# Kernel tuning notes

Measured on AMD Instinct MI355X. Metric: run time of the kernel, lower is better.

The kernel has to match this reference:

```python
import jax, jax.numpy as jnp
import numpy as np

B, T, E, H = 2, 4096, 1024, 16
D = E // H
EPS = 1e-6


def setup_inputs() -> dict:
    key = jax.random.key(0)
    ks = jax.random.split(key, 9)
    s = 1.0 / np.sqrt(E)
    return {
        "x": jax.random.normal(ks[0], (B, T, E), dtype=jnp.float32),
        "wq": jax.random.uniform(ks[1], (E, E), jnp.float32, -s, s),
        "bq": jax.random.uniform(ks[2], (E,), jnp.float32, -s, s),
        "wk": jax.random.uniform(ks[3], (E, E), jnp.float32, -s, s),
        "bk": jax.random.uniform(ks[4], (E,), jnp.float32, -s, s),
        "wv": jax.random.uniform(ks[5], (E, E), jnp.float32, -s, s),
        "bv": jax.random.uniform(ks[6], (E,), jnp.float32, -s, s),
        "wo": jax.random.uniform(ks[7], (E, E), jnp.float32, -s, s),
        "bo": jax.random.uniform(ks[8], (E,), jnp.float32, -s, s),
    }


def _feature_map(x):
    # elu(x) + 1
    return jnp.where(x > 0, x + 1.0, jnp.exp(x))


def reference(x, wq, bq, wk, bk, wv, bv, wo, bo):
    b, t, e = x.shape
    q = _feature_map(x @ wq + bq).reshape(b, t, H, D)
    k = _feature_map(x @ wk + bk).reshape(b, t, H, D)
    v = (x @ wv + bv).reshape(b, t, H, D)

    # time-major for the recurrence: [T, B, H, D]
    qT = jnp.moveaxis(q, 1, 0)
    kT = jnp.moveaxis(k, 1, 0)
    vT = jnp.moveaxis(v, 1, 0)

    S0 = jnp.zeros((b, H, D, D), dtype=x.dtype)  # running sum of k \otimes v
    z0 = jnp.zeros((b, H, D), dtype=x.dtype)     # running sum of k

    def step(carry, qkv):
        S, z = carry
        qt, kt, vt = qkv
        S = S + jnp.einsum('bhd,bhe->bhde', kt, vt)
        z = z + kt
        num = jnp.einsum('bhd,bhde->bhe', qt, S)
        den = jnp.einsum('bhd,bhd->bh', qt, z)[..., None] + EPS
        return (S, z), num / den

    _, outT = jax.lax.scan(step, (S0, z0), (qT, kT, vT))  # [T, B, H, D]
    out = jnp.moveaxis(outT, 0, 1).reshape(b, t, e)
    return out @ wo + bo
```

## Files before the change

kernel.cpp:

```cpp
#include <hip/hip_runtime.h>
#include <hip/hip_bf16.h>
#include <cstdint>
#include <cstddef>

#define B_   2
#define T_   4096
#define E_   1024
#define H_   16
#define D_   64
#define M_   (B_ * T_)
#define KDIM 1024
#define NDIM 1024
#define EPSC 1e-6f
#define CT   128
#define NC   (T_ / CT)

typedef __attribute__((ext_vector_type(8))) short bf16x8;
typedef __attribute__((ext_vector_type(4))) float f32x4;

__device__ __forceinline__ float bf2f(uint32_t u) {
    union { uint32_t u; float f; } x; x.u = u << 16; return x.f;
}
__device__ __forceinline__ unsigned short f2bf(float f) {
    union { float f; uint32_t u; } x; x.f = f;
    uint32_t r = x.u + 0x7fffu + ((x.u >> 16) & 1u);
    return (unsigned short)(r >> 16);
}
__device__ __forceinline__ void gload16(const void* g, void* l) {
    __builtin_amdgcn_global_load_lds(
        (const __attribute__((address_space(1))) void*)g,
        (__attribute__((address_space(3))) void*)l, 16, 0, 0);
}

__global__ __launch_bounds__(256) void conv_bf16(
    const float* __restrict__ in, unsigned short* __restrict__ out)
{
    const int i = blockIdx.x * 256 + threadIdx.x;
    const float4* p = (const float4*)in;
    float4 a = p[i * 2], b = p[i * 2 + 1];
    ushort4 o0 = make_ushort4(f2bf(a.x), f2bf(a.y), f2bf(a.z), f2bf(a.w));
    ushort4 o1 = make_ushort4(f2bf(b.x), f2bf(b.y), f2bf(b.z), f2bf(b.w));
    *(ushort4*)&out[(size_t)i * 8] = o0;
    *(ushort4*)&out[(size_t)i * 8 + 4] = o1;
}

__global__ __launch_bounds__(256) void transpose_w4(
    const float* __restrict__ w0, const float* __restrict__ w1,
    const float* __restrict__ w2, const float* __restrict__ w3,
    unsigned short* __restrict__ o0, unsigned short* __restrict__ o1,
    unsigned short* __restrict__ o2, unsigned short* __restrict__ o3)
{
    const float* src; unsigned short* dst;
    switch (blockIdx.z) {
        case 0: src = w0; dst = o0; break;
        case 1: src = w1; dst = o1; break;
        case 2: src = w2; dst = o2; break;
        default: src = w3; dst = o3; break;
    }
    __shared__ float tile[64][65];
    const int t = threadIdx.x, tx = t & 63, ty = t >> 6;
    const int r0 = blockIdx.y * 64, c0 = blockIdx.x * 64;
#pragma unroll
    for (int i = 0; i < 16; ++i)
        tile[ty + i * 4][tx] = src[(size_t)(r0 + ty + i * 4) * KDIM + c0 + tx];
    __syncthreads();
#pragma unroll
    for (int i = 0; i < 16; ++i)
        dst[(size_t)(c0 + ty + i * 4) * KDIM + r0 + tx] = f2bf(tile[tx][ty + i * 4]);
}

__global__ __launch_bounds__(512, 2) void gemm_qkv3(
    const unsigned short* __restrict__ A,
    const unsigned short* __restrict__ Wt,
    const float* __restrict__ bq, const float* __restrict__ bk,
    const float* __restrict__ bv,
    unsigned short* __restrict__ qb,  unsigned short* __restrict__ kb,
    unsigned short* __restrict__ ktb, unsigned short* __restrict__ vtb)
{
    __shared__ char lds[98304];

    const int tid  = threadIdx.x;
    const int lane = tid & 63;
    const int w    = tid >> 6;
    const int wm   = w >> 2;
    const int wn   = w & 3;
    const int lo   = lane & 15, hi = lane >> 4;

    const int orig = blockIdx.x;
    const int swz  = (orig & 7) * 48 + (orig >> 3);
    const int bx = swz % 12;
    const int by = swz / 12;
    const int row0 = by * 256;
    const int col0 = bx * 256;

    const unsigned short* pa0; const unsigned short* pa1;
    const unsigned short* pb0; const unsigned short* pb1;
    {
        int X, Y, r, ko;
        X = tid * 16;           Y = X ^ (((X >> 9) & 1) << 5);
        r = ((Y >> 10) << 4) + ((Y >> 6) & 15);  ko = (Y & 63) >> 1;
        pa0 = A  + (size_t)(row0 + r) * KDIM + ko;
        pb0 = Wt + (size_t)(col0 + r) * KDIM + ko;
        X = (512 + tid) * 16;   Y = X ^ (((X >> 9) & 1) << 5);
        r = ((Y >> 10) << 4) + ((Y >> 6) & 15);  ko = (Y & 63) >> 1;
        pa1 = A  + (size_t)(row0 + r) * KDIM + ko;
        pb1 = Wt + (size_t)(col0 + r) * KDIM + ko;
    }
    const int woff = w * 1024;

    const int rdb = lo * 64 + hi * 16;
    const int fragoff = rdb ^ (((rdb >> 9) & 1) << 5);

#define LDSA(b) (lds + (b) * 16384)
#define LDSB(b) (lds + 49152 + (b) * 16384)
#define STAGE_A(t, b) { gload16(pa0 + (t) * 32, LDSA(b) + woff); \
                        gload16(pa1 + (t) * 32, LDSA(b) + 8192 + woff); }
#define STAGE_B(t, b) { gload16(pb0 + (t) * 32, LDSB(b) + woff); \
                        gload16(pb1 + (t) * 32, LDSB(b) + 8192 + woff); }

    f32x4 acc[8][4] = {};
    const int NT = KDIM / 32;

    STAGE_A(0, 0); STAGE_B(0, 0);
    STAGE_A(1, 1); STAGE_B(1, 1);
    asm volatile("s_waitcnt vmcnt(4)" ::: "memory");
    __builtin_amdgcn_s_barrier();

    for (int t = 0; t < NT; ++t) {
        const int cb = t % 3;
        const char* bufA = LDSA(cb);
        const char* bufB = LDSB(cb);
        const int nb = (t + 2) % 3;
        const bool more = (t + 2 < NT);

        if (more) STAGE_A(t + 2, nb);
        bf16x8 bfr[4], af[4];
#pragma unroll
        for (int n = 0; n < 4; ++n)
            bfr[n] = *(const bf16x8*)(bufB + (wn * 4 + n) * 1024 + fragoff);
#pragma unroll
        for (int m = 0; m < 4; ++m)
            af[m] = *(const bf16x8*)(bufA + (wm * 8 + m) * 1024 + fragoff);
        asm volatile("s_waitcnt lgkmcnt(0)" ::: "memory");
        __builtin_amdgcn_sched_barrier(0);
        __builtin_amdgcn_s_setprio(1);
#pragma unroll
        for (int m = 0; m < 4; ++m)
#pragma unroll
            for (int n = 0; n < 4; ++n)
                acc[m][n] = __builtin_amdgcn_mfma_f32_16x16x32_bf16(
                    af[m], bfr[n], acc[m][n], 0, 0, 0);
        __builtin_amdgcn_s_setprio(0);

        if (more) STAGE_B(t + 2, nb);
        bf16x8 af2[4];
#pragma unroll
        for (int m = 0; m < 4; ++m)
            af2[m] = *(const bf16x8*)(bufA + (wm * 8 + 4 + m) * 1024 + fragoff);
        asm volatile("s_waitcnt lgkmcnt(0)" ::: "memory");
        __builtin_amdgcn_sched_barrier(0);
        __builtin_amdgcn_s_setprio(1);
#pragma unroll
        for (int m = 0; m < 4; ++m)
#pragma unroll
            for (int n = 0; n < 4; ++n)
                acc[4 + m][n] = __builtin_amdgcn_mfma_f32_16x16x32_bf16(
                    af2[m], bfr[n], acc[4 + m][n], 0, 0, 0);
        __builtin_amdgcn_s_setprio(0);

        if (more) asm volatile("s_waitcnt vmcnt(4)" ::: "memory");
        else      asm volatile("s_waitcnt vmcnt(0)" ::: "memory");
        __builtin_amdgcn_s_barrier();
    }
#undef STAGE_A
#undef STAGE_B
#undef LDSA
#undef LDSB

    const int matid = bx >> 2;
    const int lcol0 = (bx & 3) * 256;
    const float* bias = (matid == 0) ? bq : (matid == 1) ? bk : bv;
    const int fcol = lane & 15, frow4 = (lane >> 4) * 4;
#pragma unroll
    for (int m = 0; m < 8; ++m) {
#pragma unroll
        for (int n = 0; n < 4; ++n) {
            const int lcol = lcol0 + wn * 64 + n * 16 + fcol;
            const float bval = bias[lcol];
            const int rbase = row0 + wm * 128 + m * 16 + frow4;
            const int h = lcol >> 6, d = lcol & 63;
            const int bb = rbase >> 12;
            const int tt = rbase & (T_ - 1);
            float vv[4];
#pragma unroll
            for (int j = 0; j < 4; ++j) {
                float v = acc[m][n][j] + bval;
                if (matid <= 1) v = (v > 0.f) ? (v + 1.f) : __expf(v);
                vv[j] = v;
            }
            if (matid == 0) {
#pragma unroll
                for (int j = 0; j < 4; ++j)
                    qb[((((size_t)bb * H_ + h) * T_) + tt + j) * D_ + d] = f2bf(vv[j]);
            } else if (matid == 1) {
#pragma unroll
                for (int j = 0; j < 4; ++j)
                    kb[((((size_t)bb * H_ + h) * T_) + tt + j) * D_ + d] = f2bf(vv[j]);
                ushort4 tp = make_ushort4(f2bf(vv[0]), f2bf(vv[1]),
                                          f2bf(vv[2]), f2bf(vv[3]));
                *(ushort4*)&ktb[(((size_t)bb * H_ + h) * D_ + d) * T_ + tt] = tp;
            } else {
                ushort4 tp = make_ushort4(f2bf(vv[0]), f2bf(vv[1]),
                                          f2bf(vv[2]), f2bf(vv[3]));
                *(ushort4*)&vtb[(((size_t)bb * H_ + h) * D_ + d) * T_ + tt] = tp;
            }
        }
    }
}

__global__ __launch_bounds__(256) void gemm_out(
    const unsigned short* __restrict__ A,
    const unsigned short* __restrict__ Bt,
    const float* __restrict__ bias, float* __restrict__ outf)
{
    __shared__ unsigned short As[128 * 32];
    __shared__ unsigned short Bs[128 * 32];

    const int tid  = threadIdx.x;
    const int lane = tid & 63;
    const int wave = tid >> 6;
    const int wr = wave >> 1, wc = wave & 1;
    const int orig = blockIdx.x;
    const int swz  = (orig & 7) * 64 + (orig >> 3);
    const int bx = swz & 7, by = swz >> 3;
    const int row0 = by * 128;
    const int col0 = bx * 128;

    f32x4 acc[4][4] = {};

    const unsigned short* Ag = A  + (size_t)(row0 + (tid >> 2)) * KDIM + (tid & 3) * 8;
    const unsigned short* Bg = Bt + (size_t)(col0 + (tid >> 2)) * KDIM + (tid & 3) * 8;
    unsigned short* AsW = As + wave * 512;
    unsigned short* BsW = Bs + wave * 512;

    const int fr = lane & 15;
    const int fk = (lane >> 4) * 8;

    for (int k0 = 0; k0 < KDIM; k0 += 32) {
        gload16(Ag + k0,              AsW);
        gload16(Ag + 64 * KDIM + k0,  AsW + 2048);
        gload16(Bg + k0,              BsW);
        gload16(Bg + 64 * KDIM + k0,  BsW + 2048);
        __syncthreads();

        bf16x8 af[4], bfr[4];
#pragma unroll
        for (int m = 0; m < 4; ++m)
            af[m] = *(const bf16x8*)&As[(wr * 64 + m * 16 + fr) * 32 + fk];
#pragma unroll
        for (int n = 0; n < 4; ++n)
            bfr[n] = *(const bf16x8*)&Bs[(wc * 64 + n * 16 + fr) * 32 + fk];
#pragma unroll
        for (int m = 0; m < 4; ++m)
#pragma unroll
            for (int n = 0; n < 4; ++n)
                acc[m][n] = __builtin_amdgcn_mfma_f32_16x16x32_bf16(
                    af[m], bfr[n], acc[m][n], 0, 0, 0);
        __syncthreads();
    }

    const int fcol = lane & 15;
    const int frow = (lane >> 4) * 4;
#pragma unroll
    for (int m = 0; m < 4; ++m) {
#pragma unroll
        for (int n = 0; n < 4; ++n) {
            const int col = col0 + wc * 64 + n * 16 + fcol;
            const float bval = bias[col];
            const int rbase = row0 + wr * 64 + m * 16 + frow;
#pragma unroll
            for (int j = 0; j < 4; ++j)
                outf[(size_t)(rbase + j) * NDIM + col] = acc[m][n][j] + bval;
        }
    }
}

__global__ __launch_bounds__(256) void chunk_sums_mfma(
    const unsigned short* __restrict__ Kt,
    const unsigned short* __restrict__ Vt,
    unsigned short* __restrict__ Sl,
    unsigned short* __restrict__ Zl)
{
    const int tid = threadIdx.x, lane = tid & 63, w = tid >> 6;
    const int lo = lane & 15, hi = lane >> 4;
    const int cid = blockIdx.x, bh = cid >> 5, c = cid & 31, t0 = c * CT;
    const unsigned short* kT = Kt + (size_t)bh * 64 * T_ + t0;
    const unsigned short* vT = Vt + (size_t)bh * 64 * T_ + t0;

    const bf16x8 ones8 = {0x3F80, 0x3F80, 0x3F80, 0x3F80,
                          0x3F80, 0x3F80, 0x3F80, 0x3F80};
    f32x4 acc[5] = {};
#pragma unroll
    for (int kt = 0; kt < 4; ++kt) {
        bf16x8 af = *(const bf16x8*)&kT[(size_t)(w * 16 + lo) * T_ + kt * 32 + hi * 8];
        bf16x8 bfr[5];
#pragma unroll
        for (int et = 0; et < 4; ++et)
            bfr[et] = *(const bf16x8*)&vT[(size_t)(et * 16 + lo) * T_ + kt * 32 + hi * 8];
        bfr[4] = ones8;
#pragma unroll
        for (int et = 0; et < 5; ++et)
            acc[et] = __builtin_amdgcn_mfma_f32_16x16x32_bf16(af, bfr[et], acc[et], 0, 0, 0);
    }
    unsigned short* sO = Sl + (size_t)cid * 4096;
    const int d0 = w * 16 + hi * 4;
#pragma unroll
    for (int et = 0; et < 4; ++et) {
        const int e = et * 16 + lo;
        ushort4 pk = make_ushort4(f2bf(acc[et][0]), f2bf(acc[et][1]),
                                  f2bf(acc[et][2]), f2bf(acc[et][3]));
        *(ushort4*)&sO[e * 64 + d0] = pk;
    }
    if (lo == 0) {
        ushort4 pk = make_ushort4(f2bf(acc[4][0]), f2bf(acc[4][1]),
                                  f2bf(acc[4][2]), f2bf(acc[4][3]));
        *(ushort4*)&Zl[(size_t)cid * 64 + d0] = pk;
    }
}

__global__ __launch_bounds__(256) void chunk_scan_bf(
    unsigned short* __restrict__ S, unsigned short* __restrict__ Z)
{
    const int bh = blockIdx.y;
    const int f0 = blockIdx.x * 512 + threadIdx.x * 2;
    float a0 = 0.f, a1 = 0.f;
    unsigned short* base = S + (size_t)bh * NC * 4096 + f0;
    for (int c = 0; c < NC; ++c) {
        uint32_t* p = (uint32_t*)(base + (size_t)c * 4096);
        uint32_t v = *p;
        float c0 = bf2f(v & 0xffffu), c1 = bf2f(v >> 16);
        *p = (uint32_t)f2bf(a0) | ((uint32_t)f2bf(a1) << 16);
        a0 += c0; a1 += c1;
    }
    if (blockIdx.x == 0 && threadIdx.x < 32) {
        float b0 = 0.f, b1 = 0.f;
        unsigned short* zb = Z + (size_t)bh * NC * 64 + threadIdx.x * 2;
        for (int c = 0; c < NC; ++c) {
            uint32_t* p = (uint32_t*)(zb + (size_t)c * 64);
            uint32_t v = *p;
            float c0 = bf2f(v & 0xffffu), c1 = bf2f(v >> 16);
            *p = (uint32_t)f2bf(b0) | ((uint32_t)f2bf(b1) << 16);
            b0 += c0; b1 += c1;
        }
    }
}

__global__ __launch_bounds__(256) void chunk_attn_mfma(
    const unsigned short* __restrict__ Qb,
    const unsigned short* __restrict__ Kb,
    const unsigned short* __restrict__ Vt,
    const unsigned short* __restrict__ SpT,
    const unsigned short* __restrict__ Zp,
    unsigned short* __restrict__ att)
{
    __shared__ unsigned short lds[128 * 128];

    const int tid = threadIdx.x;
    const int lane = tid & 63;
    const int w = tid >> 6;
    const int lo = lane & 15, hi = lane >> 4;
    const int cid = blockIdx.x;
    const int bh = cid >> 5, c = cid & 31;
    const int t0 = c * CT;

    const unsigned short* qB = Qb + ((size_t)bh * T_ + t0) * 64;
    const unsigned short* kB = Kb + ((size_t)bh * T_ + t0) * 64;
    const unsigned short* vB = Vt + (size_t)bh * 64 * T_ + t0;
    const unsigned short* sB = SpT + (size_t)cid * 4096;
    const unsigned short* zB = Zp + (size_t)cid * 64;

    bf16x8 ka[2][2];
#pragma unroll
    for (int si = 0; si < 2; ++si)
#pragma unroll
        for (int kt = 0; kt < 2; ++kt)
            ka[si][kt] = *(const bf16x8*)&kB[(w * 32 + si * 16 + lo) * 64 + kt * 32 + hi * 8];

    f32x4 pacc[2][8] = {};
#pragma unroll
    for (int ti = 0; ti < 8; ++ti) {
        if (ti >= 2 * w) {
#pragma unroll
            for (int kt = 0; kt < 2; ++kt) {
                bf16x8 qf = *(const bf16x8*)&qB[(ti * 16 + lo) * 64 + kt * 32 + hi * 8];
                pacc[0][ti] = __builtin_amdgcn_mfma_f32_16x16x32_bf16(
                    ka[0][kt], qf, pacc[0][ti], 0, 0, 0);
                if (ti >= 2 * w + 1)
                    pacc[1][ti] = __builtin_amdgcn_mfma_f32_16x16x32_bf16(
                        ka[1][kt], qf, pacc[1][ti], 0, 0, 0);
            }
        }
    }
#pragma unroll
    for (int ti = 0; ti < 8; ++ti) {
        if (ti >= 2 * w) {
            const int t = ti * 16 + lo;
#pragma unroll
            for (int si = 0; si < 2; ++si) {
                const int s0 = w * 32 + si * 16 + hi * 4;
                ushort4 pk;
                unsigned short* pe = (unsigned short*)&pk;
#pragma unroll
                for (int j = 0; j < 4; ++j)
                    pe[j] = (s0 + j <= t) ? f2bf(pacc[si][ti][j]) : (unsigned short)0;
                *(ushort4*)((char*)lds + t * 256 + ((s0 * 2) ^ ((t & 7) << 4))) = pk;
            }
        }
    }
    __syncthreads();

    const bf16x8 ones8 = {0x3F80, 0x3F80, 0x3F80, 0x3F80,
                          0x3F80, 0x3F80, 0x3F80, 0x3F80};
    f32x4 acc[2][5] = {};
#pragma unroll
    for (int kt = 0; kt < 6; ++kt) {
        const int skt = kt - 2;
        if (kt < 2 || skt <= w) {
            bf16x8 bfr[5];
            if (kt < 2) {
#pragma unroll
                for (int et = 0; et < 4; ++et)
                    bfr[et] = *(const bf16x8*)&sB[(et * 16 + lo) * 64 + kt * 32 + hi * 8];
                bfr[4] = *(const bf16x8*)&zB[kt * 32 + hi * 8];
            } else {
#pragma unroll
                for (int et = 0; et < 4; ++et)
                    bfr[et] = *(const bf16x8*)&vB[(size_t)(et * 16 + lo) * T_ + skt * 32 + hi * 8];
                bfr[4] = ones8;
            }
#pragma unroll
            for (int m = 0; m < 2; ++m) {
                const int t = w * 32 + m * 16 + lo;
                bf16x8 af;
                if (kt < 2)
                    af = *(const bf16x8*)&qB[t * 64 + kt * 32 + hi * 8];
                else
                    af = *(const bf16x8*)((char*)lds + t * 256 +
                         (((skt * 32 + hi * 8) * 2) ^ ((t & 7) << 4)));
#pragma unroll
                for (int et = 0; et < 5; ++et)
                    acc[m][et] = __builtin_amdgcn_mfma_f32_16x16x32_bf16(
                        af, bfr[et], acc[m][et], 0, 0, 0);
            }
        }
    }

    __syncthreads();
#pragma unroll
    for (int m = 0; m < 2; ++m) {
#pragma unroll
        for (int j = 0; j < 4; ++j) {
            const int t = w * 32 + m * 16 + hi * 4 + j;
            const float rden = 1.f / (acc[m][4][j] + EPSC);
#pragma unroll
            for (int et = 0; et < 4; ++et) {
                const int e = et * 16 + lo;
                *(unsigned short*)((char*)lds + t * 144 + e * 2) =
                    f2bf(acc[m][et][j] * rden);
            }
        }
    }
    __syncthreads();
    const int b = bh >> 4, h = bh & 15;
#pragma unroll
    for (int r = 0; r < 4; ++r) {
        const int vid = tid + r * 256;
        const int t = vid >> 3, eg = vid & 7;
        uint4 val = *(const uint4*)((const char*)lds + t * 144 + eg * 16);
        *(uint4*)&att[(size_t)(b * T_ + t0 + t) * E_ + h * 64 + eg * 8] = val;
    }
}

extern "C" void kernel_launch(void* const* d_in, const int* in_sizes, int n_in,
                              void* d_out, int out_size, void* d_ws, size_t ws_size,
                              hipStream_t stream)
{
    const float* x  = (const float*)d_in[0];
    const float* wq = (const float*)d_in[1];
    const float* bq = (const float*)d_in[2];
    const float* wk = (const float*)d_in[3];
    const float* bk = (const float*)d_in[4];
    const float* wv = (const float*)d_in[5];
    const float* bv = (const float*)d_in[6];
    const float* wo = (const float*)d_in[7];
    const float* bo = (const float*)d_in[8];
    float* out = (float*)d_out;

    char* ws = (char*)d_ws;
    unsigned short* qb  = (unsigned short*)(ws);
    unsigned short* kb  = (unsigned short*)(ws + (size_t)16 * 1024 * 1024);
    unsigned short* ktb = (unsigned short*)(ws + (size_t)32 * 1024 * 1024);
    unsigned short* vtb = (unsigned short*)(ws + (size_t)48 * 1024 * 1024);
    unsigned short* xb  = (unsigned short*)(ws + (size_t)64 * 1024 * 1024);
    unsigned short* attb = xb;
    unsigned short* Sl  = (unsigned short*)(ws + (size_t)80 * 1024 * 1024);
    unsigned short* Zl  = (unsigned short*)(ws + (size_t)88 * 1024 * 1024);
    unsigned short* wqT = (unsigned short*)(ws + (size_t)88 * 1024 * 1024 + 128 * 1024);
    unsigned short* wkT = wqT + (size_t)KDIM * NDIM;
    unsigned short* wvT = wkT + (size_t)KDIM * NDIM;
    unsigned short* woT = wvT + (size_t)KDIM * NDIM;

    conv_bf16<<<M_ * KDIM / (256 * 8), 256, 0, stream>>>(x, xb);
    transpose_w4<<<dim3(16, 16, 4), 256, 0, stream>>>(wq, wk, wv, wo,
                                                      wqT, wkT, wvT, woT);

    gemm_qkv3<<<384, 512, 0, stream>>>(xb, wqT, bq, bk, bv, qb, kb, ktb, vtb);

    chunk_sums_mfma<<<B_ * H_ * NC, 256, 0, stream>>>(ktb, vtb, Sl, Zl);
    chunk_scan_bf<<<dim3(8, B_ * H_), 256, 0, stream>>>(Sl, Zl);
    chunk_attn_mfma<<<B_ * H_ * NC, 256, 0, stream>>>(qb, kb, vtb, Sl, Zl, attb);

    gemm_out<<<512, 256, 0, stream>>>(attb, woT, bo, out);
}
```

Before: 171.1 us.

## Rework QKV GEMM mainloop to K=64 double-buffered tiles with interleaved prefetch

Restructures the fused QKV projection GEMM to process K in steps of 64 instead of 32, using two 64 KB double buffers (128 KB LDS) in place of a 3-stage ring of 32-wide tiles. The LDS layout changes to 128-byte rows with an XOR swizzle on bank-conflicting bits. The global-to-LDS loads for the next B tile and the A tile two steps ahead are split into halves and interleaved between four MFMA groups. The aim is to halve the per-K-step barrier and waitcnt overhead and hide load latency better. It raises LDS use to 128 KB per block, which may limit occupancy to one block per CU despite launch_bounds(512,2), and adds an extra mid-iteration barrier.

```diff
diff --git a/kernel.cpp b/kernel.cpp
--- a/kernel.cpp
+++ b/kernel.cpp
@@ -69,7 +69,7 @@
         dst[(size_t)(c0 + ty + i * 4) * KDIM + r0 + tx] = f2bf(tile[tx][ty + i * 4]);
 }
 
-__global__ __launch_bounds__(512, 2) void gemm_qkv3(
+__global__ __launch_bounds__(512, 2) void gemm_qkv8(
     const unsigned short* __restrict__ A,
     const unsigned short* __restrict__ Wt,
     const float* __restrict__ bq, const float* __restrict__ bk,
@@ -77,7 +77,7 @@
     unsigned short* __restrict__ qb,  unsigned short* __restrict__ kb,
     unsigned short* __restrict__ ktb, unsigned short* __restrict__ vtb)
 {
-    __shared__ char lds[98304];
+    __shared__ char lds[131072];
 
     const int tid  = threadIdx.x;
     const int lane = tid & 63;
@@ -93,99 +93,115 @@
     const int row0 = by * 256;
     const int col0 = bx * 256;
 
-    const unsigned short* pa0; const unsigned short* pa1;
-    const unsigned short* pb0; const unsigned short* pb1;
-    {
-        int X, Y, r, ko;
-        X = tid * 16;           Y = X ^ (((X >> 9) & 1) << 5);
-        r = ((Y >> 10) << 4) + ((Y >> 6) & 15);  ko = (Y & 63) >> 1;
-        pa0 = A  + (size_t)(row0 + r) * KDIM + ko;
-        pb0 = Wt + (size_t)(col0 + r) * KDIM + ko;
-        X = (512 + tid) * 16;   Y = X ^ (((X >> 9) & 1) << 5);
-        r = ((Y >> 10) << 4) + ((Y >> 6) & 15);  ko = (Y & 63) >> 1;
-        pa1 = A  + (size_t)(row0 + r) * KDIM + ko;
-        pb1 = Wt + (size_t)(col0 + r) * KDIM + ko;
-    }
-    const int woff = w * 1024;
-
-    const int rdb = lo * 64 + hi * 16;
-    const int fragoff = rdb ^ (((rdb >> 9) & 1) << 5);
-
-#define LDSA(b) (lds + (b) * 16384)
-#define LDSB(b) (lds + 49152 + (b) * 16384)
-#define STAGE_A(t, b) { gload16(pa0 + (t) * 32, LDSA(b) + woff); \
-                        gload16(pa1 + (t) * 32, LDSA(b) + 8192 + woff); }
-#define STAGE_B(t, b) { gload16(pb0 + (t) * 32, LDSB(b) + woff); \
-                        gload16(pb1 + (t) * 32, LDSB(b) + 8192 + woff); }
-
-    f32x4 acc[8][4] = {};
-    const int NT = KDIM / 32;
-
-    STAGE_A(0, 0); STAGE_B(0, 0);
-    STAGE_A(1, 1); STAGE_B(1, 1);
+    int sr0, sk0, sr1, sk1;
+    { int X = tid * 16;         int Y = X ^ (((X >> 7) & 7) << 4);
+      sr0 = Y >> 7; sk0 = (Y & 127) >> 1; }
+    { int X = (512 + tid) * 16; int Y = X ^ (((X >> 7) & 7) << 4);
+      sr1 = Y >> 7; sk1 = (Y & 127) >> 1; }
+    const unsigned short* sA0 = A  + (size_t)(row0 + sr0) * KDIM + sk0;
+    const unsigned short* sA1 = A  + (size_t)(row0 + sr1) * KDIM + sk1;
+    const unsigned short* sB0 = Wt + (size_t)(col0 + sr0) * KDIM + sk0;
+    const unsigned short* sB1 = Wt + (size_t)(col0 + sr1) * KDIM + sk1;
+
+#define BUFA(p) (lds + (p) * 32768)
+#define BUFB(p) (lds + 65536 + (p) * 32768)
+#define STGA(t, h) { char* d_ = BUFA((t) & 1) + (h) * 16384 + w * 1024;      \
+        gload16(sA0 + (size_t)(h) * 128 * KDIM + (t) * 64, d_);              \
+        gload16(sA1 + (size_t)(h) * 128 * KDIM + (t) * 64, d_ + 8192); }
+#define STGB(t, h) { char* d_ = BUFB((t) & 1) + (h) * 16384 + w * 1024;      \
+        gload16(sB0 + (size_t)(h) * 128 * KDIM + (t) * 64, d_);              \
+        gload16(sB1 + (size_t)(h) * 128 * KDIM + (t) * 64, d_ + 8192); }
+
+    const int koff0 = (hi * 16)      ^ ((lane & 7) << 4);
+    const int koff1 = (64 + hi * 16) ^ ((lane & 7) << 4);
+
+    f32x4  acc[8][4] = {};
+    bf16x8 af[8][2], bfr[4][2];
+
+#define MFMA_PAIR(mb) {                                                       \
+    _Pragma("unroll") for (int kk = 0; kk < 2; ++kk)                          \
+    _Pragma("unroll") for (int n = 0; n < 4; ++n) {                           \
+        acc[mb][n]     = __builtin_amdgcn_mfma_f32_16x16x32_bf16(             \
+            af[mb][kk],     bfr[n][kk], acc[mb][n], 0, 0, 0);                 \
+        acc[mb + 1][n] = __builtin_amdgcn_mfma_f32_16x16x32_bf16(             \
+            af[mb + 1][kk], bfr[n][kk], acc[mb + 1][n], 0, 0, 0);             \
+    } }
+
+    STGA(0, 0); STGA(0, 1); STGB(0, 0); STGB(0, 1);
+    STGA(1, 0); STGA(1, 1);
     asm volatile("s_waitcnt vmcnt(4)" ::: "memory");
     __builtin_amdgcn_s_barrier();
 
+    const int NT = KDIM / 64;
+#pragma unroll 2
     for (int t = 0; t < NT; ++t) {
-        const int cb = t % 3;
-        const char* bufA = LDSA(cb);
-        const char* bufB = LDSB(cb);
-        const int nb = (t + 2) % 3;
-        const bool more = (t + 2 < NT);
-
-        if (more) STAGE_A(t + 2, nb);
-        bf16x8 bfr[4], af[4];
-#pragma unroll
-        for (int n = 0; n < 4; ++n)
-            bfr[n] = *(const bf16x8*)(bufB + (wn * 4 + n) * 1024 + fragoff);
-#pragma unroll
-        for (int m = 0; m < 4; ++m)
-            af[m] = *(const bf16x8*)(bufA + (wm * 8 + m) * 1024 + fragoff);
+        const char* bA = BUFA(t & 1);
+        const char* bB = BUFB(t & 1);
+
+        if (t + 1 < NT) STGB(t + 1, 0);
+#pragma unroll
+        for (int n = 0; n < 4; ++n) {
+            const char* p = bB + (wn * 64 + n * 16 + lo) * 128;
+            bfr[n][0] = *(const bf16x8*)(p + koff0);
+            bfr[n][1] = *(const bf16x8*)(p + koff1);
+        }
+#pragma unroll
+        for (int m = 0; m < 2; ++m) {
+            const char* p = bA + (wm * 128 + m * 16 + lo) * 128;
+            af[m][0] = *(const bf16x8*)(p + koff0);
+            af[m][1] = *(const bf16x8*)(p + koff1);
+        }
         asm volatile("s_waitcnt lgkmcnt(0)" ::: "memory");
         __builtin_amdgcn_sched_barrier(0);
         __builtin_amdgcn_s_setprio(1);
-#pragma unroll
-        for (int m = 0; m < 4; ++m)
-#pragma unroll
-            for (int n = 0; n < 4; ++n)
-                acc[m][n] = __builtin_amdgcn_mfma_f32_16x16x32_bf16(
-                    af[m], bfr[n], acc[m][n], 0, 0, 0);
+        MFMA_PAIR(0);
         __builtin_amdgcn_s_setprio(0);
-
-        if (more) STAGE_B(t + 2, nb);
-        bf16x8 af2[4];
-#pragma unroll
-        for (int m = 0; m < 4; ++m)
-            af2[m] = *(const bf16x8*)(bufA + (wm * 8 + 4 + m) * 1024 + fragoff);
+        __builtin_amdgcn_sched_barrier(0);
+
+        if (t + 1 < NT) STGB(t + 1, 1);
+#pragma unroll
+        for (int m = 2; m < 8; ++m) {
+            const char* p = bA + (wm * 128 + m * 16 + lo) * 128;
+            af[m][0] = *(const bf16x8*)(p + koff0);
+            af[m][1] = *(const bf16x8*)(p + koff1);
+        }
         asm volatile("s_waitcnt lgkmcnt(0)" ::: "memory");
         __builtin_amdgcn_sched_barrier(0);
+        __builtin_amdgcn_s_barrier();
         __builtin_amdgcn_s_setprio(1);
-#pragma unroll
-        for (int m = 0; m < 4; ++m)
-#pragma unroll
-            for (int n = 0; n < 4; ++n)
-                acc[4 + m][n] = __builtin_amdgcn_mfma_f32_16x16x32_bf16(
-                    af2[m], bfr[n], acc[4 + m][n], 0, 0, 0);
+        MFMA_PAIR(2);
         __builtin_amdgcn_s_setprio(0);
-
-        if (more) asm volatile("s_waitcnt vmcnt(4)" ::: "memory");
-        else      asm volatile("s_waitcnt vmcnt(0)" ::: "memory");
+        __builtin_amdgcn_sched_barrier(0);
+
+        if (t + 2 < NT) STGA(t + 2, 0);
+        __builtin_amdgcn_s_setprio(1);
+        MFMA_PAIR(4);
+        __builtin_amdgcn_s_setprio(0);
+        __builtin_amdgcn_sched_barrier(0);
+
+        if (t + 2 < NT) STGA(t + 2, 1);
+        __builtin_amdgcn_s_setprio(1);
+        MFMA_PAIR(6);
+        __builtin_amdgcn_s_setprio(0);
+        if (t + 2 < NT) asm volatile("s_waitcnt vmcnt(4)" ::: "memory");
+        else            asm volatile("s_waitcnt vmcnt(0)" ::: "memory");
         __builtin_amdgcn_s_barrier();
     }
-#undef STAGE_A
-#undef STAGE_B
-#undef LDSA
-#undef LDSB
+#undef STGA
+#undef STGB
+#undef BUFA
+#undef BUFB
+#undef MFMA_PAIR
 
     const int matid = bx >> 2;
     const int lcol0 = (bx & 3) * 256;
     const float* bias = (matid == 0) ? bq : (matid == 1) ? bk : bv;
-    const int fcol = lane & 15, frow4 = (lane >> 4) * 4;
+    const int frow4 = hi * 4;
 #pragma unroll
     for (int m = 0; m < 8; ++m) {
 #pragma unroll
         for (int n = 0; n < 4; ++n) {
-            const int lcol = lcol0 + wn * 64 + n * 16 + fcol;
+            const int lcol = lcol0 + wn * 64 + n * 16 + lo;
             const float bval = bias[lcol];
             const int rbase = row0 + wm * 128 + m * 16 + frow4;
             const int h = lcol >> 6, d = lcol & 63;
@@ -514,7 +530,7 @@
     transpose_w4<<<dim3(16, 16, 4), 256, 0, stream>>>(wq, wk, wv, wo,
                                                       wqT, wkT, wvT, woT);
 
-    gemm_qkv3<<<384, 512, 0, stream>>>(xb, wqT, bq, bk, bv, qb, kb, ktb, vtb);
+    gemm_qkv8<<<384, 512, 0, stream>>>(xb, wqT, bq, bk, bv, qb, kb, ktb, vtb);
 
     chunk_sums_mfma<<<B_ * H_ * NC, 256, 0, stream>>>(ktb, vtb, Sl, Zl);
     chunk_scan_bf<<<dim3(8, B_ * H_), 256, 0, stream>>>(Sl, Zl);
```

After: 165.9 us. 1.03x faster.
